# Kernel optimization log

Hardware: AMD Instinct MI355X
Metric: run time of the kernel (lower is better)

The kernel has to match this reference:

```python
import jax, jax.numpy as jnp
import numpy as np

NUM_HEADS = 16
HEAD_DIM = 64  # att_output_dim // num_heads = 1024 // 16


def setup_inputs() -> dict:
    key = jax.random.key(0)
    ks = jax.random.split(key, 7)
    B, S, D_IN, D_OUT = 4, 2048, 1024, 1024
    std = 1.0 / np.sqrt(D_IN)
    return {
        "ts10_input": jax.random.normal(ks[0], (B, S, D_IN), dtype=jnp.float32),
        "Wq": jax.random.uniform(ks[1], (D_IN, D_OUT), jnp.float32, -std, std),
        "bq": jax.random.uniform(ks[2], (D_OUT,), jnp.float32, -std, std),
        "Wk": jax.random.uniform(ks[3], (D_IN, D_OUT), jnp.float32, -std, std),
        "bk": jax.random.uniform(ks[4], (D_OUT,), jnp.float32, -std, std),
        "Wv": jax.random.uniform(ks[5], (D_IN, D_OUT), jnp.float32, -std, std),
        "bv": jax.random.uniform(ks[6], (D_OUT,), jnp.float32, -std, std),
        "mask": 1,
    }


def reference(ts10_input, Wq, bq, Wk, bk, Wv, bv, mask):
    B, S, _ = ts10_input.shape
    H, Dh = NUM_HEADS, HEAD_DIM

    def split_heads(x):  # (B,S,H*Dh) -> (B,H,S,Dh)
        return x.reshape(B, S, H, Dh).transpose(0, 2, 1, 3)

    q = split_heads(ts10_input @ Wq + bq)
    k = split_heads(ts10_input @ Wk + bk)
    v = split_heads(ts10_input @ Wv + bv)

    scores = jnp.einsum("bhqd,bhkd->bhqk", q, k) / jnp.sqrt(jnp.float32(Dh))
    if mask:
        causal = jnp.tril(jnp.ones((S, S), dtype=bool))  # keep lower triangle incl diag
        scores = jnp.where(causal, scores, -jnp.inf)
    probs = jax.nn.softmax(scores, axis=-1)
    ctx = jnp.einsum("bhqk,bhkd->bhqd", probs, v)
    return ctx.transpose(0, 2, 1, 3).reshape(B, S, H * Dh)
```

## Files before the change

### kernel.cpp

```cpp
#include <hip/hip_runtime.h>

typedef __bf16 bf16x8 __attribute__((ext_vector_type(8)));
typedef __bf16 bf16x4 __attribute__((ext_vector_type(4)));
typedef short s16x4 __attribute__((ext_vector_type(4)));
typedef float f32x4 __attribute__((ext_vector_type(4)));
typedef unsigned short u16x8 __attribute__((ext_vector_type(8)));
typedef unsigned short u16x4 __attribute__((ext_vector_type(4)));
typedef unsigned int u32x2 __attribute__((ext_vector_type(2)));
typedef unsigned int __attribute__((address_space(1))) as1_uint;
typedef unsigned int __attribute__((address_space(3))) as3_uint;

#define S_LEN 2048
#define NB 4
#define NH 16
#define HD 64
#define DM 1024

#define Q_SCALE 0.18033688011112042f

__device__ __forceinline__ unsigned short f2bf(float f) {
  union { float f; unsigned int u; } v; v.f = f;
  unsigned int r = v.u + 0x7fffu + ((v.u >> 16) & 1u);
  return (unsigned short)(r >> 16);
}

__device__ __forceinline__ unsigned int fbits(float f) {
  union { float f; unsigned int u; } v; v.f = f;
  return v.u;
}

__device__ __forceinline__ f32x4 mfma16(u16x4 a, u16x4 b, f32x4 c) {
#if __has_builtin(__builtin_amdgcn_mfma_f32_16x16x16_bf16)
  return __builtin_amdgcn_mfma_f32_16x16x16_bf16(
      __builtin_bit_cast(bf16x4, a), __builtin_bit_cast(bf16x4, b), c, 0, 0, 0);
#else
  return __builtin_amdgcn_mfma_f32_16x16x16bf16_1k(
      __builtin_bit_cast(s16x4, a), __builtin_bit_cast(s16x4, b), c, 0, 0, 0);
#endif
}

__global__ __launch_bounds__(256) void cvt_x(const float* __restrict__ x,
                                             unsigned short* __restrict__ xb) {
  int i = (blockIdx.x * 256 + threadIdx.x) * 8;
  f32x4 a = *(const f32x4*)(x + i);
  f32x4 b = *(const f32x4*)(x + i + 4);
  u16x8 o;
  o[0] = f2bf(a[0]); o[1] = f2bf(a[1]); o[2] = f2bf(a[2]); o[3] = f2bf(a[3]);
  o[4] = f2bf(b[0]); o[5] = f2bf(b[1]); o[6] = f2bf(b[2]); o[7] = f2bf(b[3]);
  *(u16x8*)(xb + i) = o;
}

__global__ __launch_bounds__(256) void cvt_wt(const float* __restrict__ Wq,
                                              const float* __restrict__ Wk,
                                              const float* __restrict__ Wv,
                                              unsigned short* __restrict__ wt) {
  const float* W = (blockIdx.z == 0) ? Wq : (blockIdx.z == 1) ? Wk : Wv;
  unsigned short* WT = wt + (size_t)blockIdx.z * DM * DM;
  __shared__ float tile[32][33];
  int tx = threadIdx.x & 31, ty = threadIdx.x >> 5;
  int k0 = blockIdx.x * 32, n0 = blockIdx.y * 32;
#pragma unroll
  for (int i = 0; i < 4; ++i)
    tile[ty + 8 * i][tx] = W[(size_t)(k0 + ty + 8 * i) * DM + n0 + tx];
  __syncthreads();
#pragma unroll
  for (int i = 0; i < 4; ++i)
    WT[(size_t)(n0 + ty + 8 * i) * DM + k0 + tx] = f2bf(tile[tx][ty + 8 * i]);
}

__global__ __launch_bounds__(256) void qkv_gemm(const unsigned short* __restrict__ xb,
                                                const unsigned short* __restrict__ wt,
                                                const float* __restrict__ bq,
                                                const float* __restrict__ bk,
                                                const float* __restrict__ bv,
                                                unsigned short* __restrict__ qo,
                                                unsigned short* __restrict__ ko,
                                                unsigned short* __restrict__ vto) {
  const int z = blockIdx.z;
  const unsigned short* WT = wt + (size_t)z * DM * DM;
  const float* bias = (z == 0) ? bq : (z == 1) ? bk : bv;
  const int m0 = blockIdx.x * 128;
  const int n0 = blockIdx.y * 128;
  __shared__ __align__(16) unsigned short Al[128 * 32];
  __shared__ __align__(16) unsigned short Bl[128 * 32];
  const int tid = threadIdx.x;
  const int wave = tid >> 6, lane = tid & 63, quad = lane >> 4, lw = lane & 15;
  const int wm = (wave >> 1) * 64, wn = (wave & 1) * 64;

  f32x4 acc[4][4];
#pragma unroll
  for (int mt = 0; mt < 4; ++mt)
#pragma unroll
    for (int nt = 0; nt < 4; ++nt) acc[mt][nt] = (f32x4){0.f, 0.f, 0.f, 0.f};

  for (int k0 = 0; k0 < DM; k0 += 32) {
    __syncthreads();
#pragma unroll
    for (int i = 0; i < 2; ++i) {
      int c = i * 256 + tid;
      int row = c >> 2;
      int scn = (c & 3) ^ ((row >> 1) & 3);
      const unsigned short* ga = xb + (size_t)(m0 + row) * DM + k0 + scn * 8;
      __builtin_amdgcn_global_load_lds((const as1_uint*)ga, (as3_uint*)(Al + c * 8), 16, 0, 0);
      const unsigned short* gb = WT + (size_t)(n0 + row) * DM + k0 + scn * 8;
      __builtin_amdgcn_global_load_lds((const as1_uint*)gb, (as3_uint*)(Bl + c * 8), 16, 0, 0);
    }
    __syncthreads();
    bf16x8 af[4], bfr[4];
#pragma unroll
    for (int mt = 0; mt < 4; ++mt) {
      int r = wm + mt * 16 + lw;
      af[mt] = *(const bf16x8*)(Al + r * 32 + (quad ^ ((r >> 1) & 3)) * 8);
    }
#pragma unroll
    for (int nt = 0; nt < 4; ++nt) {
      int r = wn + nt * 16 + lw;
      bfr[nt] = *(const bf16x8*)(Bl + r * 32 + (quad ^ ((r >> 1) & 3)) * 8);
    }
#pragma unroll
    for (int mt = 0; mt < 4; ++mt)
#pragma unroll
      for (int nt = 0; nt < 4; ++nt)
        acc[mt][nt] = __builtin_amdgcn_mfma_f32_16x16x32_bf16(af[mt], bfr[nt], acc[mt][nt], 0, 0, 0);
  }

  float bias4[4];
#pragma unroll
  for (int nt = 0; nt < 4; ++nt) bias4[nt] = bias[n0 + wn + nt * 16 + lw];

  if (z < 2) {
    unsigned short* dst = (z == 0) ? qo : ko;
    const float sc = (z == 0) ? Q_SCALE : 1.0f;
#pragma unroll
    for (int mt = 0; mt < 4; ++mt) {
#pragma unroll
      for (int nt = 0; nt < 4; ++nt) {
        int n = n0 + wn + nt * 16 + lw;
        int h = n >> 6, d = n & 63;
#pragma unroll
        for (int r = 0; r < 4; ++r) {
          int m = m0 + wm + mt * 16 + quad * 4 + r;
          int b = m >> 11, s = m & 2047;
          dst[((size_t)(b * NH + h) * S_LEN + s) * HD + d] = f2bf((acc[mt][nt][r] + bias4[nt]) * sc);
        }
      }
    }
  } else {
#pragma unroll
    for (int mt = 0; mt < 4; ++mt) {
#pragma unroll
      for (int nt = 0; nt < 4; ++nt) {
        int n = n0 + wn + nt * 16 + lw;
        int h = n >> 6, d = n & 63;
        int mb = m0 + wm + mt * 16 + quad * 4;
        int b = mb >> 11, s = mb & 2047;
        u16x4 pk;
#pragma unroll
        for (int r = 0; r < 4; ++r) pk[r] = f2bf(acc[mt][nt][r] + bias4[nt]);
        *(u16x4*)(vto + ((size_t)(b * NH + h) * HD + d) * S_LEN + s) = pk;
      }
    }
  }
}

__global__ __launch_bounds__(256, 4) void attn(const unsigned short* __restrict__ Qb,
                                               const unsigned short* __restrict__ Kb,
                                               const unsigned short* __restrict__ Vtb,
                                               float* __restrict__ out) {
  const int flat = blockIdx.x;
  const int bh_lo = flat & 7;
  const int qpair = (flat >> 3) & 15;
  const int bh_hi = flat >> 7;
  const int bh = bh_lo + 8 * bh_hi;
  const int b = bh >> 4, h = bh & 15;
  const int tid = threadIdx.x;
  const int wave = tid >> 6, lane = tid & 63;
  const int quad = lane >> 4, lw = lane & 15;
  const int qlo = qpair * 64;
  const int qhi = (31 - qpair) * 64;
  const unsigned short* Qp = Qb + (size_t)bh * S_LEN * HD;
  const unsigned short* Kp = Kb + (size_t)bh * S_LEN * HD;
  const unsigned short* Vp = Vtb + (size_t)bh * HD * S_LEN;

  __shared__ __align__(16) unsigned short Kl[2][64 * 64];
  __shared__ __align__(16) unsigned short Vl[2][64 * 64];

  bf16x8 aq[2][2];
#pragma unroll
  for (int rg = 0; rg < 2; ++rg) {
    const int qbase = rg ? qhi : qlo;
#pragma unroll
    for (int kc = 0; kc < 2; ++kc)
      aq[rg][kc] = *(const bf16x8*)(Qp + (size_t)(qbase + wave * 16 + lw) * HD + kc * 32 + quad * 8);
  }

  u16x4 ones4;
#pragma unroll
  for (int i = 0; i < 4; ++i) ones4[i] = 0x3F80;

  f32x4 accO[2][4];
  f32x4 accL[2];
#pragma unroll
  for (int rg = 0; rg < 2; ++rg) {
    accL[rg] = (f32x4){0.f, 0.f, 0.f, 0.f};
#pragma unroll
    for (int dg = 0; dg < 4; ++dg) accO[rg][dg] = (f32x4){0.f, 0.f, 0.f, 0.f};
  }

  const int qr0 = qlo + wave * 16 + lw;
  const int qr1 = qhi + wave * 16 + lw;

  const int T = 32 - qpair;

  {
#pragma unroll
    for (int i = 0; i < 2; ++i) {
      int idx = i * 256 + tid;
      int r = idx >> 3, c = (idx & 7) ^ (r & 7);
      __builtin_amdgcn_global_load_lds((const as1_uint*)(Kp + (size_t)r * HD + c * 8),
                                       (as3_uint*)(Kl[0] + idx * 8), 16, 0, 0);
      __builtin_amdgcn_global_load_lds((const as1_uint*)(Vp + (size_t)r * S_LEN + c * 8),
                                       (as3_uint*)(Vl[0] + idx * 8), 16, 0, 0);
    }
  }

  for (int t = 0; t < T; ++t) {
    const int kv = t * 64;
    const int cur = t & 1;
    __syncthreads();

    if (t + 1 < T) {
      const int kvn = kv + 64;
#pragma unroll
      for (int i = 0; i < 2; ++i) {
        int idx = i * 256 + tid;
        int r = idx >> 3, c = (idx & 7) ^ (r & 7);
        __builtin_amdgcn_global_load_lds((const as1_uint*)(Kp + (size_t)(kvn + r) * HD + c * 8),
                                         (as3_uint*)(Kl[cur ^ 1] + idx * 8), 16, 0, 0);
        __builtin_amdgcn_global_load_lds((const as1_uint*)(Vp + (size_t)r * S_LEN + kvn + c * 8),
                                         (as3_uint*)(Vl[cur ^ 1] + idx * 8), 16, 0, 0);
      }
    }

    const bool a0 = (t <= qpair);
    const bool d0 = (t == qpair);
    const bool d1 = (t == T - 1);

#pragma unroll
    for (int g = 0; g < 4; ++g) {
      const unsigned short* kp = Kl[cur] + (g * 16 + lw) * 64;
      const int sw = lw & 7;
      bf16x8 kf0 = *(const bf16x8*)(kp + ((quad ^ sw) * 8));
      bf16x8 kf1 = *(const bf16x8*)(kp + (((4 + quad) ^ sw) * 8));

      u16x4 pf[2];
#pragma unroll
      for (int rg = 0; rg < 2; ++rg) {
        if (rg == 0 && !a0) continue;
        f32x4 s = (f32x4){0.f, 0.f, 0.f, 0.f};
        s = __builtin_amdgcn_mfma_f32_16x16x32_bf16(kf0, aq[rg][0], s, 0, 0, 0);
        s = __builtin_amdgcn_mfma_f32_16x16x32_bf16(kf1, aq[rg][1], s, 0, 0, 0);
        const bool dg_ = rg ? d1 : d0;
        const int qr = rg ? qr1 : qr0;
        if (dg_) {
#pragma unroll
          for (int r = 0; r < 4; ++r) {
            float e = __builtin_amdgcn_exp2f(s[r]);
            s[r] = (kv + g * 16 + quad * 4 + r > qr) ? 0.f : e;
          }
        } else {
#pragma unroll
          for (int r = 0; r < 4; ++r) s[r] = __builtin_amdgcn_exp2f(s[r]);
        }
        u32x2 pk;
        pk[0] = (fbits(s[1]) & 0xFFFF0000u) | (fbits(s[0]) >> 16);
        pk[1] = (fbits(s[3]) & 0xFFFF0000u) | (fbits(s[2]) >> 16);
        pf[rg] = __builtin_bit_cast(u16x4, pk);
      }

#pragma unroll
      for (int dg = 0; dg < 4; ++dg) {
        const int row = dg * 16 + lw;
        const int slot = (2 * g + (quad >> 1)) ^ (lw & 7);
        u16x4 vf = *(const u16x4*)(Vl[cur] + row * 64 + slot * 8 + (quad & 1) * 4);
        if (a0) accO[0][dg] = mfma16(pf[0], vf, accO[0][dg]);
        accO[1][dg] = mfma16(pf[1], vf, accO[1][dg]);
      }
      if (a0) accL[0] = mfma16(pf[0], ones4, accL[0]);
      accL[1] = mfma16(pf[1], ones4, accL[1]);
    }
  }

#pragma unroll
  for (int rg = 0; rg < 2; ++rg) {
    const int qbase = rg ? qhi : qlo;
    float* op = out + ((size_t)b * S_LEN + qbase + wave * 16 + quad * 4) * DM + h * HD + lw;
#pragma unroll
    for (int r = 0; r < 4; ++r) {
      float inv = 1.0f / accL[rg][r];
#pragma unroll
      for (int dg = 0; dg < 4; ++dg) op[(size_t)r * DM + dg * 16] = accO[rg][dg][r] * inv;
    }
  }
}

extern "C" void kernel_launch(void* const* d_in, const int* in_sizes, int n_in,
                              void* d_out, int out_size, void* d_ws, size_t ws_size,
                              hipStream_t stream) {
  const float* x = (const float*)d_in[0];
  const float* Wq = (const float*)d_in[1];
  const float* bq = (const float*)d_in[2];
  const float* Wk = (const float*)d_in[3];
  const float* bk = (const float*)d_in[4];
  const float* Wv = (const float*)d_in[5];
  const float* bv = (const float*)d_in[6];
  float* out = (float*)d_out;

  char* ws = (char*)d_ws;
  unsigned short* xb = (unsigned short*)(ws + 0);
  unsigned short* wt = (unsigned short*)(ws + 16777216);
  unsigned short* qb = (unsigned short*)(ws + 23068672);
  unsigned short* kb = (unsigned short*)(ws + 39845888);
  unsigned short* vt = (unsigned short*)(ws + 56623104);

  hipLaunchKernelGGL(cvt_x, dim3(4096), dim3(256), 0, stream, x, xb);
  hipLaunchKernelGGL(cvt_wt, dim3(32, 32, 3), dim3(256), 0, stream, Wq, Wk, Wv, wt);
  hipLaunchKernelGGL(qkv_gemm, dim3(64, 8, 3), dim3(256), 0, stream,
                     xb, wt, bq, bk, bv, qb, kb, vt);
  hipLaunchKernelGGL(attn, dim3(1024), dim3(256), 0, stream, qb, kb, vt, out);
}
```

Baseline: 225.0 us.

## Double-buffer LDS tiles in QKV GEMM to overlap global loads with MFMA

Result: no change. 222.8 us (-1.0%).

```diff
diff --git a/kernel.cpp b/kernel.cpp
--- a/kernel.cpp
+++ b/kernel.cpp
@@ -81,8 +81,8 @@
   const float* bias = (z == 0) ? bq : (z == 1) ? bk : bv;
   const int m0 = blockIdx.x * 128;
   const int n0 = blockIdx.y * 128;
-  __shared__ __align__(16) unsigned short Al[128 * 32];
-  __shared__ __align__(16) unsigned short Bl[128 * 32];
+  __shared__ __align__(16) unsigned short Al[2][128 * 32];
+  __shared__ __align__(16) unsigned short Bl[2][128 * 32];
   const int tid = threadIdx.x;
   const int wave = tid >> 6, lane = tid & 63, quad = lane >> 4, lw = lane & 15;
   const int wm = (wave >> 1) * 64, wn = (wave & 1) * 64;
@@ -93,29 +93,45 @@
 #pragma unroll
     for (int nt = 0; nt < 4; ++nt) acc[mt][nt] = (f32x4){0.f, 0.f, 0.f, 0.f};
 
+#pragma unroll
+  for (int i = 0; i < 2; ++i) {
+    int c = i * 256 + tid;
+    int row = c >> 2;
+    int scn = (c & 3) ^ ((row >> 1) & 3);
+    const unsigned short* ga = xb + (size_t)(m0 + row) * DM + scn * 8;
+    __builtin_amdgcn_global_load_lds((const as1_uint*)ga, (as3_uint*)(Al[0] + c * 8), 16, 0, 0);
+    const unsigned short* gb = WT + (size_t)(n0 + row) * DM + scn * 8;
+    __builtin_amdgcn_global_load_lds((const as1_uint*)gb, (as3_uint*)(Bl[0] + c * 8), 16, 0, 0);
+  }
+
   for (int k0 = 0; k0 < DM; k0 += 32) {
+    const int cur = (k0 >> 5) & 1;
     __syncthreads();
-#pragma unroll
-    for (int i = 0; i < 2; ++i) {
-      int c = i * 256 + tid;
-      int row = c >> 2;
-      int scn = (c & 3) ^ ((row >> 1) & 3);
-      const unsigned short* ga = xb + (size_t)(m0 + row) * DM + k0 + scn * 8;
-      __builtin_amdgcn_global_load_lds((const as1_uint*)ga, (as3_uint*)(Al + c * 8), 16, 0, 0);
-      const unsigned short* gb = WT + (size_t)(n0 + row) * DM + k0 + scn * 8;
-      __builtin_amdgcn_global_load_lds((const as1_uint*)gb, (as3_uint*)(Bl + c * 8), 16, 0, 0);
-    }
-    __syncthreads();
+
+    if (k0 + 32 < DM) {
+      const int kn = k0 + 32;
+#pragma unroll
+      for (int i = 0; i < 2; ++i) {
+        int c = i * 256 + tid;
+        int row = c >> 2;
+        int scn = (c & 3) ^ ((row >> 1) & 3);
+        const unsigned short* ga = xb + (size_t)(m0 + row) * DM + kn + scn * 8;
+        __builtin_amdgcn_global_load_lds((const as1_uint*)ga, (as3_uint*)(Al[cur ^ 1] + c * 8), 16, 0, 0);
+        const unsigned short* gb = WT + (size_t)(n0 + row) * DM + kn + scn * 8;
+        __builtin_amdgcn_global_load_lds((const as1_uint*)gb, (as3_uint*)(Bl[cur ^ 1] + c * 8), 16, 0, 0);
+      }
+    }
+
     bf16x8 af[4], bfr[4];
 #pragma unroll
     for (int mt = 0; mt < 4; ++mt) {
       int r = wm + mt * 16 + lw;
-      af[mt] = *(const bf16x8*)(Al + r * 32 + (quad ^ ((r >> 1) & 3)) * 8);
+      af[mt] = *(const bf16x8*)(Al[cur] + r * 32 + (quad ^ ((r >> 1) & 3)) * 8);
     }
 #pragma unroll
     for (int nt = 0; nt < 4; ++nt) {
       int r = wn + nt * 16 + lw;
-      bfr[nt] = *(const bf16x8*)(Bl + r * 32 + (quad ^ ((r >> 1) & 3)) * 8);
+      bfr[nt] = *(const bf16x8*)(Bl[cur] + r * 32 + (quad ^ ((r >> 1) & 3)) * 8);
     }
 #pragma unroll
     for (int mt = 0; mt < 4; ++mt)
```

## Triple-buffer QKV GEMM with larger tiles and deeper K steps

Applied to the files above, without the earlier changes.

Result: no change. 221.9 us (-1.4%).

```diff
diff --git a/kernel.cpp b/kernel.cpp
--- a/kernel.cpp
+++ b/kernel.cpp
@@ -68,21 +68,23 @@
     WT[(size_t)(n0 + ty + 8 * i) * DM + k0 + tx] = f2bf(tile[tx][ty + 8 * i]);
 }
 
-__global__ __launch_bounds__(256) void qkv_gemm(const unsigned short* __restrict__ xb,
-                                                const unsigned short* __restrict__ wt,
-                                                const float* __restrict__ bq,
-                                                const float* __restrict__ bk,
-                                                const float* __restrict__ bv,
-                                                unsigned short* __restrict__ qo,
-                                                unsigned short* __restrict__ ko,
-                                                unsigned short* __restrict__ vto) {
+#define QKV_LDS_BYTES 147456
+__global__ __launch_bounds__(512, 2) void qkv_gemm(const unsigned short* __restrict__ xb,
+                                                   const unsigned short* __restrict__ wt,
+                                                   const float* __restrict__ bq,
+                                                   const float* __restrict__ bk,
+                                                   const float* __restrict__ bv,
+                                                   unsigned short* __restrict__ qo,
+                                                   unsigned short* __restrict__ ko,
+                                                   unsigned short* __restrict__ vto) {
+  extern __shared__ char smem_dyn[];
+  unsigned short* As = (unsigned short*)smem_dyn;
+  unsigned short* Bs = As + 3 * 256 * 64;
   const int z = blockIdx.z;
   const unsigned short* WT = wt + (size_t)z * DM * DM;
   const float* bias = (z == 0) ? bq : (z == 1) ? bk : bv;
-  const int m0 = blockIdx.x * 128;
+  const int m0 = blockIdx.x * 256;
   const int n0 = blockIdx.y * 128;
-  __shared__ __align__(16) unsigned short Al[128 * 32];
-  __shared__ __align__(16) unsigned short Bl[128 * 32];
   const int tid = threadIdx.x;
   const int wave = tid >> 6, lane = tid & 63, quad = lane >> 4, lw = lane & 15;
   const int wm = (wave >> 1) * 64, wn = (wave & 1) * 64;
@@ -93,35 +95,67 @@
 #pragma unroll
     for (int nt = 0; nt < 4; ++nt) acc[mt][nt] = (f32x4){0.f, 0.f, 0.f, 0.f};
 
-  for (int k0 = 0; k0 < DM; k0 += 32) {
-    __syncthreads();
+  auto stage = [&](int tile) {
+    const int kt = tile * 64;
+    const int bsel = tile % 3;
+    unsigned short* Ad = As + bsel * (256 * 64);
+    unsigned short* Bd = Bs + bsel * (128 * 64);
+#pragma unroll
+    for (int i = 0; i < 4; ++i) {
+      int c = i * 512 + tid;
+      int row = c >> 3, scn = (c & 7) ^ (row & 7);
+      __builtin_amdgcn_global_load_lds((const as1_uint*)(xb + (size_t)(m0 + row) * DM + kt + scn * 8),
+                                       (as3_uint*)(Ad + c * 8), 16, 0, 0);
+    }
 #pragma unroll
     for (int i = 0; i < 2; ++i) {
-      int c = i * 256 + tid;
-      int row = c >> 2;
-      int scn = (c & 3) ^ ((row >> 1) & 3);
-      const unsigned short* ga = xb + (size_t)(m0 + row) * DM + k0 + scn * 8;
-      __builtin_amdgcn_global_load_lds((const as1_uint*)ga, (as3_uint*)(Al + c * 8), 16, 0, 0);
-      const unsigned short* gb = WT + (size_t)(n0 + row) * DM + k0 + scn * 8;
-      __builtin_amdgcn_global_load_lds((const as1_uint*)gb, (as3_uint*)(Bl + c * 8), 16, 0, 0);
-    }
-    __syncthreads();
-    bf16x8 af[4], bfr[4];
-#pragma unroll
-    for (int mt = 0; mt < 4; ++mt) {
-      int r = wm + mt * 16 + lw;
-      af[mt] = *(const bf16x8*)(Al + r * 32 + (quad ^ ((r >> 1) & 3)) * 8);
-    }
-#pragma unroll
-    for (int nt = 0; nt < 4; ++nt) {
-      int r = wn + nt * 16 + lw;
-      bfr[nt] = *(const bf16x8*)(Bl + r * 32 + (quad ^ ((r >> 1) & 3)) * 8);
-    }
-#pragma unroll
-    for (int mt = 0; mt < 4; ++mt)
-#pragma unroll
-      for (int nt = 0; nt < 4; ++nt)
-        acc[mt][nt] = __builtin_amdgcn_mfma_f32_16x16x32_bf16(af[mt], bfr[nt], acc[mt][nt], 0, 0, 0);
+      int c = i * 512 + tid;
+      int row = c >> 3, scn = (c & 7) ^ (row & 7);
+      __builtin_amdgcn_global_load_lds((const as1_uint*)(WT + (size_t)(n0 + row) * DM + kt + scn * 8),
+                                       (as3_uint*)(Bd + c * 8), 16, 0, 0);
+    }
+  };
+
+  stage(0);
+  stage(1);
+  asm volatile("s_waitcnt vmcnt(6)" ::: "memory");
+  __builtin_amdgcn_s_barrier();
+  asm volatile("" ::: "memory");
+
+#pragma unroll
+  for (int t = 0; t < 16; ++t) {
+    if (t + 2 < 16) stage(t + 2);
+
+    const unsigned short* Ab = As + (t % 3) * (256 * 64);
+    const unsigned short* Bb = Bs + (t % 3) * (128 * 64);
+    bf16x8 af[2][4], bfq[2][4];
+#pragma unroll
+    for (int k = 0; k < 2; ++k) {
+#pragma unroll
+      for (int mt = 0; mt < 4; ++mt) {
+        int r = wm + mt * 16 + lw;
+        af[k][mt] = *(const bf16x8*)(Ab + r * 64 + (((k * 4 + quad) ^ (r & 7)) * 8));
+      }
+#pragma unroll
+      for (int nt = 0; nt < 4; ++nt) {
+        int r = wn + nt * 16 + lw;
+        bfq[k][nt] = *(const bf16x8*)(Bb + r * 64 + (((k * 4 + quad) ^ (r & 7)) * 8));
+      }
+    }
+#pragma unroll
+    for (int k = 0; k < 2; ++k)
+#pragma unroll
+      for (int mt = 0; mt < 4; ++mt)
+#pragma unroll
+        for (int nt = 0; nt < 4; ++nt)
+          acc[mt][nt] = __builtin_amdgcn_mfma_f32_16x16x32_bf16(af[k][mt], bfq[k][nt], acc[mt][nt], 0, 0, 0);
+
+    if (t < 15) {
+      if (t < 14) asm volatile("s_waitcnt vmcnt(6)" ::: "memory");
+      else        asm volatile("s_waitcnt vmcnt(0)" ::: "memory");
+      __builtin_amdgcn_s_barrier();
+      asm volatile("" ::: "memory");
+    }
   }
 
   float bias4[4];
@@ -323,9 +357,12 @@
   unsigned short* kb = (unsigned short*)(ws + 39845888);
   unsigned short* vt = (unsigned short*)(ws + 56623104);
 
+  hipFuncSetAttribute((const void*)qkv_gemm,
+                      hipFuncAttributeMaxDynamicSharedMemorySize, QKV_LDS_BYTES);
+
   hipLaunchKernelGGL(cvt_x, dim3(4096), dim3(256), 0, stream, x, xb);
   hipLaunchKernelGGL(cvt_wt, dim3(32, 32, 3), dim3(256), 0, stream, Wq, Wk, Wv, wt);
-  hipLaunchKernelGGL(qkv_gemm, dim3(64, 8, 3), dim3(256), 0, stream,
+  hipLaunchKernelGGL(qkv_gemm, dim3(32, 8, 3), dim3(512), QKV_LDS_BYTES, stream,
                      xb, wt, bq, bk, bv, qb, kb, vt);
   hipLaunchKernelGGL(attn, dim3(1024), dim3(256), 0, stream, qb, kb, vt, out);
 }
```
